# Kernel tuning notes

Measured on AMD Instinct MI355X. Metric: run time of the kernel, lower is better.

## Reference

```python
import jax, jax.numpy as jnp
import numpy as np

HEADS = 12
DIM = 768


def setup_inputs() -> dict:
    key = jax.random.key(0)
    ks = jax.random.split(key, 4)
    s = 0.02
    return {
        "x": jax.random.normal(ks[0], (8, 64, 64, DIM), dtype=jnp.float32),
        "w_qkv_h": jax.random.normal(ks[1], (DIM, 3 * DIM), dtype=jnp.float32) * s,
        "b_qkv_h": jnp.zeros((3 * DIM,), jnp.float32),
        "w_qkv_w": jax.random.normal(ks[2], (DIM, 3 * DIM), dtype=jnp.float32) * s,
        "b_qkv_w": jnp.zeros((3 * DIM,), jnp.float32),
        "w_proj": jax.random.normal(ks[3], (DIM, DIM), dtype=jnp.float32) * s,
        "b_proj": jnp.zeros((DIM,), jnp.float32),
    }


def _axial_attn(x_seq, w, b, heads, scale):
    # x_seq: [N, L, C]. Faithful to original torch code: q,k,v keep shape
    # [N, L, heads, hd]; matmul contracts hd, producing [N, L, heads, heads]
    # attention ACROSS HEADS at each position (no head permute in the source).
    N, L, C = x_seq.shape
    hd = C // heads
    qkv = (x_seq @ w + b).reshape(N, L, 3, heads, hd)
    q = qkv[:, :, 0] * scale
    k = qkv[:, :, 1]
    v = qkv[:, :, 2]
    attn = jax.nn.softmax(jnp.einsum('nlhd,nlgd->nlhg', q, k), axis=-1)
    out = jnp.einsum('nlhg,nlgd->nlhd', attn, v)
    return out.reshape(N, L, C)


def reference(x, w_qkv_h, b_qkv_h, w_qkv_w, b_qkv_w, w_proj, b_proj):
    B, H, W, C = x.shape
    scale = (C // HEADS) ** -0.5
    # H-axis pass: permute to [B, W, H, C], flatten batch*W
    x_h = jnp.transpose(x, (0, 2, 1, 3)).reshape(B * W, H, C)
    out_h = _axial_attn(x_h, w_qkv_h, b_qkv_h, HEADS, scale)
    out_h = jnp.transpose(out_h.reshape(B, W, H, C), (0, 2, 1, 3))
    # W-axis pass: flatten batch*H
    out_w = _axial_attn(x.reshape(B * H, W, C), w_qkv_w, b_qkv_w, HEADS, scale)
    out_w = out_w.reshape(B, H, W, C)
    # residual-style sum of the two axes, then output projection (dropout p=0)
    return (out_h + out_w) @ w_proj + b_proj
```

## Files before the change

### kernel.cpp

```cpp
#include <hip/hip_runtime.h>

typedef unsigned short u16;
typedef unsigned int u32;
typedef __attribute__((ext_vector_type(8))) short short8;
typedef __attribute__((ext_vector_type(4))) float f32x4;

#define DIMC 768
#define NQKV 2304
#define NPOS 32768
#define NKT 12

__device__ __forceinline__ float b2f(u16 u) {
    union { u32 i; float f; } c; c.i = ((u32)u) << 16; return c.f;
}
__device__ __forceinline__ u16 f2b(float f) {
    union { float f; u32 i; } c; c.f = f;
    u32 r = c.i + 0x7fffu + ((c.i >> 16) & 1u);
    return (u16)(r >> 16);
}

__device__ __forceinline__ void gl_lds16(const void* g, void* l) {
    __builtin_amdgcn_global_load_lds(
        (const __attribute__((address_space(1))) void*)g,
        (__attribute__((address_space(3))) void*)l, 16, 0, 0);
}

__global__ __launch_bounds__(256) void cvt_bf16(
    const float* __restrict__ in, u16* __restrict__ out, int n4)
{
    int i = blockIdx.x * 256 + threadIdx.x;
    if (i >= n4) return;
    float4 v = ((const float4*)in)[i];
    ushort4 o;
    o.x = f2b(v.x); o.y = f2b(v.y); o.z = f2b(v.z); o.w = f2b(v.w);
    ((ushort4*)out)[i] = o;
}

__global__ __launch_bounds__(256) void cvt_wT(
    const float* __restrict__ W0, const float* __restrict__ W1,
    const float* __restrict__ W2,
    u16* __restrict__ T0, u16* __restrict__ T1, u16* __restrict__ T2)
{
    const int z = blockIdx.z;
    const float* W = (z == 0) ? W0 : (z == 1) ? W1 : W2;
    u16* WT = (z == 0) ? T0 : (z == 1) ? T1 : T2;
    const int N = (z == 2) ? 768 : 2304;
    const int nb = blockIdx.x, kb = blockIdx.y;
    if (nb * 64 >= N) return;
    __shared__ u16 T[64][65];
    const int t = threadIdx.x, sr = t >> 2, sc = t & 3;
    {
        const float4* p = (const float4*)(W + (size_t)(kb * 64 + sr) * N + nb * 64 + sc * 16);
        float4 a0 = p[0], a1 = p[1], a2 = p[2], a3 = p[3];
        float vv[16] = {a0.x, a0.y, a0.z, a0.w, a1.x, a1.y, a1.z, a1.w,
                        a2.x, a2.y, a2.z, a2.w, a3.x, a3.y, a3.z, a3.w};
        #pragma unroll
        for (int i = 0; i < 16; ++i)
            T[sc * 16 + i][sr] = f2b(vv[i]);
    }
    __syncthreads();
    {
        u16 vv[16];
        #pragma unroll
        for (int i = 0; i < 16; ++i) vv[i] = T[sr][sc * 16 + i];
        uint4 p0, p1;
        p0.x = vv[0] | ((u32)vv[1] << 16);  p0.y = vv[2] | ((u32)vv[3] << 16);
        p0.z = vv[4] | ((u32)vv[5] << 16);  p0.w = vv[6] | ((u32)vv[7] << 16);
        p1.x = vv[8] | ((u32)vv[9] << 16);  p1.y = vv[10] | ((u32)vv[11] << 16);
        p1.z = vv[12] | ((u32)vv[13] << 16); p1.w = vv[14] | ((u32)vv[15] << 16);
        u16* q = WT + (size_t)(nb * 64 + sr) * DIMC + kb * 64 + sc * 16;
        *(uint4*)q = p0;
        *(uint4*)(q + 8) = p1;
    }
}


#define STAGE_A(buf, kt, ht) do {                                              \
    gl_lds16(aS + (size_t)((ht) * 128)      * DIMC + (size_t)(kt) * 64,        \
             &As[buf][(ht) * 8192 +        w * 512]);                          \
    gl_lds16(aS + (size_t)((ht) * 128 + 64) * DIMC + (size_t)(kt) * 64,        \
             &As[buf][(ht) * 8192 + 4096 + w * 512]);                          \
} while (0)

#define STAGE_B(buf, kt, ht) do {                                              \
    gl_lds16(bS + (size_t)((ht) * 128)      * DIMC + (size_t)(kt) * 64,        \
             &Bs[buf][(ht) * 8192 +        w * 512]);                          \
    gl_lds16(bS + (size_t)((ht) * 128 + 64) * DIMC + (size_t)(kt) * 64,        \
             &Bs[buf][(ht) * 8192 + 4096 + w * 512]);                          \
} while (0)

#define READ_A(base, hm) do {                                                  \
    _Pragma("unroll")                                                          \
    for (int i_ = 0; i_ < 4; ++i_) {                                           \
        const int row_ = (hm) * 128 + wm * 64 + i_ * 16 + lr;                  \
        _Pragma("unroll")                                                      \
        for (int ks_ = 0; ks_ < 2; ++ks_)                                      \
            af[i_][ks_] = *(const short8*)((base) + (row_ << 6) +              \
                              (((ks_ * 4 + lq) ^ (row_ & 7)) << 3));           \
    }                                                                          \
} while (0)

#define READ_B(dst, base, hn) do {                                             \
    _Pragma("unroll")                                                          \
    for (int j_ = 0; j_ < 2; ++j_) {                                           \
        const int row_ = (hn) * 128 + wn * 32 + j_ * 16 + lr;                  \
        _Pragma("unroll")                                                      \
        for (int ks_ = 0; ks_ < 2; ++ks_)                                      \
            (dst)[j_][ks_] = *(const short8*)((base) + (row_ << 6) +           \
                              (((ks_ * 4 + lq) ^ (row_ & 7)) << 3));           \
    }                                                                          \
} while (0)

#define MM(hm, hn, bsrc) do {                                                  \
    __builtin_amdgcn_s_setprio(1);                                             \
    _Pragma("unroll")                                                          \
    for (int i_ = 0; i_ < 4; ++i_)                                             \
        _Pragma("unroll")                                                      \
        for (int j_ = 0; j_ < 2; ++j_)                                         \
            _Pragma("unroll")                                                  \
            for (int ks_ = 0; ks_ < 2; ++ks_)                                  \
                acc[(hm) * 4 + i_][(hn) * 2 + j_] =                            \
                    __builtin_amdgcn_mfma_f32_16x16x32_bf16(                   \
                        af[i_][ks_], (bsrc)[j_][ks_],                          \
                        acc[(hm) * 4 + i_][(hn) * 2 + j_], 0, 0, 0);           \
    __builtin_amdgcn_s_setprio(0);                                             \
} while (0)

#define BAR() do {                                                             \
    __builtin_amdgcn_sched_barrier(0);                                         \
    __builtin_amdgcn_s_barrier();                                              \
    __builtin_amdgcn_sched_barrier(0);                                         \
} while (0)

#define KTILE(kt, S12, S34, VN) do {                                           \
    const int p_ = (kt) & 1, q_ = p_ ^ 1;                                      \
    const u16* Ab_ = As[p_];                                                   \
    const u16* Bb_ = Bs[p_];                                                   \
                                                             \
    READ_A(Ab_, 0);                                                            \
    READ_B(b0, Bb_, 0);                                                        \
    if (S12) STAGE_B(q_, (kt) + 1, 1);                                         \
    BAR();                                                                     \
    MM(0, 0, b0);                                                              \
                                                             \
    READ_B(b1, Bb_, 1);                                                        \
    if (S12) STAGE_A(q_, (kt) + 1, 1);                                         \
    BAR();                                                                     \
    MM(0, 1, b1);                                                              \
                                                             \
    READ_A(Ab_, 1);                                                            \
    if (S34) STAGE_A(p_, (kt) + 2, 0);                                         \
    BAR();                                                                     \
    MM(1, 0, b0);                                                              \
                                                             \
    if (S34) STAGE_B(p_, (kt) + 2, 0);                                         \
    __builtin_amdgcn_sched_barrier(0);                                         \
    asm volatile("s_waitcnt vmcnt(" VN ")" ::: "memory");                      \
    BAR();                                                                     \
    MM(1, 1, b1);                                                              \
} while (0)

__global__ __launch_bounds__(512, 2) void gemm256(
    const u16* __restrict__ A, const u16* __restrict__ BT,
    const float* __restrict__ bias, void* __restrict__ C,
    int ldn, int c_is_f32)
{
    __shared__ __align__(16) u16 As[2][256 * 64];
    __shared__ __align__(16) u16 Bs[2][256 * 64];

    const int t = threadIdx.x;
    const int w = t >> 6, l = t & 63;
    const int wm = w >> 2, wn = w & 3;
    const int lr = l & 15, lq = l >> 4;

    const int gx = (int)gridDim.x;
    const int nwg = gx * (int)gridDim.y;
    const int lin = (int)blockIdx.y * gx + (int)blockIdx.x;
    const int swz = (lin & 7) * (nwg >> 3) + (lin >> 3);
    const int by = swz / gx, bx = swz - by * gx;
    const int mBase = by * 256, nBase = bx * 256;

    const int srow = t >> 3;
    const int schk = (t & 7) ^ (srow & 7);
    const u16* aS = A  + (size_t)(mBase + srow) * DIMC + schk * 8;
    const u16* bS = BT + (size_t)(nBase + srow) * DIMC + schk * 8;

    f32x4 acc[8][4];
    #pragma unroll
    for (int i = 0; i < 8; ++i)
        #pragma unroll
        for (int j = 0; j < 4; ++j)
            acc[i][j] = (f32x4){0.f, 0.f, 0.f, 0.f};

    short8 af[4][2], b0[2][2], b1[2][2];

    STAGE_A(0, 0, 0); STAGE_B(0, 0, 0); STAGE_B(0, 0, 1); STAGE_A(0, 0, 1);
    STAGE_A(1, 1, 0); STAGE_B(1, 1, 0);
    __builtin_amdgcn_sched_barrier(0);
    asm volatile("s_waitcnt vmcnt(4)" ::: "memory");
    BAR();

    #pragma unroll 1
    for (int kt = 0; kt < NKT - 2; ++kt) { KTILE(kt, 1, 1, "4"); }
    { KTILE(NKT - 2, 1, 0, "0"); }
    { KTILE(NKT - 1, 0, 0, "0"); }

    #pragma unroll
    for (int hn = 0; hn < 2; ++hn)
        #pragma unroll
        for (int j = 0; j < 2; ++j) {
            const int col = nBase + hn * 128 + wn * 32 + j * 16 + lr;
            const float bb = bias[col];
            #pragma unroll
            for (int hm = 0; hm < 2; ++hm)
                #pragma unroll
                for (int i = 0; i < 4; ++i) {
                    const int row = mBase + hm * 128 + wm * 64 + i * 16 + lq * 4;
                    #pragma unroll
                    for (int rg = 0; rg < 4; ++rg) {
                        float v = acc[hm * 4 + i][hn * 2 + j][rg] + bb;
                        size_t idx = (size_t)(row + rg) * ldn + col;
                        if (c_is_f32) ((float*)C)[idx] = v;
                        else          ((u16*)C)[idx]   = f2b(v);
                    }
                }
        }
}

__global__ __launch_bounds__(256) void headattn(
    const u16* __restrict__ qkv, u16* __restrict__ sum, int accumulate)
{
    __shared__ u16 VtL[4][64 * 16];
    __shared__ u16 PL[4][16 * 16];
    const int t = threadIdx.x, wv = t >> 6, l = t & 63;
    const int p = blockIdx.x * 4 + wv;
    const u16* row = qkv + (size_t)p * NQKV;
    const int lr = l & 15, lq = l >> 4;
    u16* Vt = VtL[wv];
    u16* P  = PL[wv];

    short8 qa0 = *(const short8*)(row +       lr * 64 + lq * 8);
    short8 qa1 = *(const short8*)(row +       lr * 64 + lq * 8 + 32);
    short8 kb0 = *(const short8*)(row + 768 + lr * 64 + lq * 8);
    short8 kb1 = *(const short8*)(row + 768 + lr * 64 + lq * 8 + 32);

    *(uint2*)(Vt + l * 16 + 12) = (uint2){0u, 0u};
    {
        const int g = l >> 3, d0 = (l & 7) * 8;
        short8 v = *(const short8*)(row + 1536 + g * 64 + d0);
        #pragma unroll
        for (int i = 0; i < 8; ++i) Vt[(d0 + i) * 16 + g] = (u16)v[i];
        if (l < 32) {
            const int g2 = 8 + (l >> 3);
            short8 v2 = *(const short8*)(row + 1536 + g2 * 64 + d0);
            #pragma unroll
            for (int i = 0; i < 8; ++i) Vt[(d0 + i) * 16 + g2] = (u16)v2[i];
        }
    }

    f32x4 s = (f32x4){0.f, 0.f, 0.f, 0.f};
    s = __builtin_amdgcn_mfma_f32_16x16x32_bf16(qa0, kb0, s, 0, 0, 0);
    s = __builtin_amdgcn_mfma_f32_16x16x32_bf16(qa1, kb1, s, 0, 0, 0);

    #pragma unroll
    for (int rg = 0; rg < 4; ++rg) {
        float x = (lr < 12) ? s[rg] * 0.125f : -1e30f;
        float m = x;
        m = fmaxf(m, __shfl_xor(m, 1));
        m = fmaxf(m, __shfl_xor(m, 2));
        m = fmaxf(m, __shfl_xor(m, 4));
        m = fmaxf(m, __shfl_xor(m, 8));
        float e = (lr < 12) ? __expf(x - m) : 0.f;
        float ss = e;
        ss += __shfl_xor(ss, 1);
        ss += __shfl_xor(ss, 2);
        ss += __shfl_xor(ss, 4);
        ss += __shfl_xor(ss, 8);
        P[(lq * 4 + rg) * 16 + lr] = f2b(e / ss);
    }

    const short8 z8 = (short8){0, 0, 0, 0, 0, 0, 0, 0};
    short8 pa = z8;
    if (lq < 2) pa = *(const short8*)(P + lr * 16 + lq * 8);
    f32x4 o[4];
    #pragma unroll
    for (int c = 0; c < 4; ++c) {
        short8 vb = z8;
        if (lq < 2) vb = *(const short8*)(Vt + (c * 16 + lr) * 16 + lq * 8);
        f32x4 a0 = (f32x4){0.f, 0.f, 0.f, 0.f};
        o[c] = __builtin_amdgcn_mfma_f32_16x16x32_bf16(pa, vb, a0, 0, 0, 0);
    }

    if (lq < 3) {
        u16* orow = sum + (size_t)p * DIMC;
        #pragma unroll
        for (int c = 0; c < 4; ++c)
            #pragma unroll
            for (int rg = 0; rg < 4; ++rg) {
                const int idx = (lq * 4 + rg) * 64 + c * 16 + lr;
                float v = o[c][rg];
                if (accumulate) v += b2f(orow[idx]);
                orow[idx] = f2b(v);
            }
    }
}

extern "C" void kernel_launch(void* const* d_in, const int* in_sizes, int n_in,
                              void* d_out, int out_size, void* d_ws, size_t ws_size,
                              hipStream_t stream) {
    const float* x  = (const float*)d_in[0];
    const float* wh = (const float*)d_in[1];
    const float* bh = (const float*)d_in[2];
    const float* ww = (const float*)d_in[3];
    const float* bw = (const float*)d_in[4];
    const float* wp = (const float*)d_in[5];
    const float* bp = (const float*)d_in[6];
    float* out = (float*)d_out;

    u16* xb   = (u16*)d_ws;
    u16* whT  = xb   + 25165824;
    u16* wwT  = whT  + 1769472;
    u16* wpT  = wwT  + 1769472;
    u16* qkvb = wpT  + 589824;
    u16* sumb = qkvb + 75497472;

    cvt_bf16<<<24576, 256, 0, stream>>>(x, xb, 6291456);
    dim3 wg(36, 12, 3);
    cvt_wT<<<wg, 256, 0, stream>>>(wh, ww, wp, whT, wwT, wpT);

    dim3 gq(NQKV / 256, NPOS / 256);
    dim3 gp(DIMC / 256, NPOS / 256);

    gemm256<<<gq, 512, 0, stream>>>(xb, whT, bh, qkvb, NQKV, 0);
    headattn<<<NPOS / 4, 256, 0, stream>>>(qkvb, sumb, 0);
    gemm256<<<gq, 512, 0, stream>>>(xb, wwT, bw, qkvb, NQKV, 0);
    headattn<<<NPOS / 4, 256, 0, stream>>>(qkvb, sumb, 1);
    gemm256<<<gp, 512, 0, stream>>>(sumb, wpT, bp, out, DIMC, 1);
}
```

Measured before the change: 585.1 us.

## Fuse both axial attention passes into one kernel and prefetch GEMM fragments

The two per-position head-attention launches are merged into one kernel that reads both QKV buffers, sums both outputs in registers and writes the bf16 sum once. This removes the read-modify-write of the sum buffer and one launch. The P·V product now runs on VALU FMAs with shuffles instead of MFMA through LDS. The GEMM main loop double-buffers its A fragments and loads the next tile's A/B fragments during the last MFMA block, hiding LDS latency at the cost of more registers. A second QKV buffer is allocated, and the sum reuses the x bf16 buffer.

```diff
diff --git a/kernel.cpp b/kernel.cpp
--- a/kernel.cpp
+++ b/kernel.cpp
@@ -89,13 +89,13 @@
              &Bs[buf][(ht) * 8192 + 4096 + w * 512]);                          \
 } while (0)
 
-#define READ_A(base, hm) do {                                                  \
+#define READ_A(dst, base, hm) do {                                             \
     _Pragma("unroll")                                                          \
     for (int i_ = 0; i_ < 4; ++i_) {                                           \
         const int row_ = (hm) * 128 + wm * 64 + i_ * 16 + lr;                  \
         _Pragma("unroll")                                                      \
         for (int ks_ = 0; ks_ < 2; ++ks_)                                      \
-            af[i_][ks_] = *(const short8*)((base) + (row_ << 6) +              \
+            (dst)[i_][ks_] = *(const short8*)((base) + (row_ << 6) +           \
                               (((ks_ * 4 + lq) ^ (row_ & 7)) << 3));           \
     }                                                                          \
 } while (0)
@@ -111,7 +111,7 @@
     }                                                                          \
 } while (0)
 
-#define MM(hm, hn, bsrc) do {                                                  \
+#define MM(hm, hn, asrc, bsrc) do {                                            \
     __builtin_amdgcn_s_setprio(1);                                             \
     _Pragma("unroll")                                                          \
     for (int i_ = 0; i_ < 4; ++i_)                                             \
@@ -121,7 +121,7 @@
             for (int ks_ = 0; ks_ < 2; ++ks_)                                  \
                 acc[(hm) * 4 + i_][(hn) * 2 + j_] =                            \
                     __builtin_amdgcn_mfma_f32_16x16x32_bf16(                   \
-                        af[i_][ks_], (bsrc)[j_][ks_],                          \
+                        (asrc)[i_][ks_], (bsrc)[j_][ks_],                      \
                         acc[(hm) * 4 + i_][(hn) * 2 + j_], 0, 0, 0);           \
     __builtin_amdgcn_s_setprio(0);                                             \
 } while (0)
@@ -132,32 +132,29 @@
     __builtin_amdgcn_sched_barrier(0);                                         \
 } while (0)
 
-#define KTILE(kt, S12, S34, VN) do {                                           \
+#define KTILE(kt, S12, S34, SNEXT, VN) do {                                    \
     const int p_ = (kt) & 1, q_ = p_ ^ 1;                                      \
-    const u16* Ab_ = As[p_];                                                   \
-    const u16* Bb_ = Bs[p_];                                                   \
                                                              \
-    READ_A(Ab_, 0);                                                            \
-    READ_B(b0, Bb_, 0);                                                        \
     if (S12) STAGE_B(q_, (kt) + 1, 1);                                         \
+    READ_B(b1, Bs[p_], 1);                                                     \
     BAR();                                                                     \
-    MM(0, 0, b0);                                                              \
+    MM(0, 0, af_a, b0);                                                        \
                                                              \
-    READ_B(b1, Bb_, 1);                                                        \
     if (S12) STAGE_A(q_, (kt) + 1, 1);                                         \
+    READ_A(af_b, As[p_], 1);                                                   \
     BAR();                                                                     \
-    MM(0, 1, b1);                                                              \
+    MM(0, 1, af_a, b1);                                                        \
                                                              \
-    READ_A(Ab_, 1);                                                            \
     if (S34) STAGE_A(p_, (kt) + 2, 0);                                         \
     BAR();                                                                     \
-    MM(1, 0, b0);                                                              \
+    MM(1, 0, af_b, b0);                                                        \
                                                              \
     if (S34) STAGE_B(p_, (kt) + 2, 0);                                         \
     __builtin_amdgcn_sched_barrier(0);                                         \
     asm volatile("s_waitcnt vmcnt(" VN ")" ::: "memory");                      \
     BAR();                                                                     \
-    MM(1, 1, b1);                                                              \
+    if (SNEXT) { READ_A(af_a, As[q_], 0); READ_B(b0, Bs[q_], 0); }             \
+    MM(1, 1, af_b, b1);                                                        \
 } while (0)
 
 __global__ __launch_bounds__(512, 2) void gemm256(
@@ -192,18 +189,20 @@
         for (int j = 0; j < 4; ++j)
             acc[i][j] = (f32x4){0.f, 0.f, 0.f, 0.f};
 
-    short8 af[4][2], b0[2][2], b1[2][2];
+    short8 af_a[4][2], af_b[4][2], b0[2][2], b1[2][2];
 
     STAGE_A(0, 0, 0); STAGE_B(0, 0, 0); STAGE_B(0, 0, 1); STAGE_A(0, 0, 1);
     STAGE_A(1, 1, 0); STAGE_B(1, 1, 0);
     __builtin_amdgcn_sched_barrier(0);
     asm volatile("s_waitcnt vmcnt(4)" ::: "memory");
     BAR();
+    READ_A(af_a, As[0], 0);
+    READ_B(b0, Bs[0], 0);
 
     #pragma unroll 1
-    for (int kt = 0; kt < NKT - 2; ++kt) { KTILE(kt, 1, 1, "4"); }
-    { KTILE(NKT - 2, 1, 0, "0"); }
-    { KTILE(NKT - 1, 0, 0, "0"); }
+    for (int kt = 0; kt < NKT - 2; ++kt) { KTILE(kt, 1, 1, 1, "4"); }
+    { KTILE(NKT - 2, 1, 0, 1, "0"); }
+    { KTILE(NKT - 1, 0, 0, 0, "0"); }
 
     #pragma unroll
     for (int hn = 0; hn < 2; ++hn)
@@ -227,41 +226,14 @@
         }
 }
 
-__global__ __launch_bounds__(256) void headattn(
-    const u16* __restrict__ qkv, u16* __restrict__ sum, int accumulate)
-{
-    __shared__ u16 VtL[4][64 * 16];
-    __shared__ u16 PL[4][16 * 16];
-    const int t = threadIdx.x, wv = t >> 6, l = t & 63;
-    const int p = blockIdx.x * 4 + wv;
-    const u16* row = qkv + (size_t)p * NQKV;
-    const int lr = l & 15, lq = l >> 4;
-    u16* Vt = VtL[wv];
-    u16* P  = PL[wv];
-
-    short8 qa0 = *(const short8*)(row +       lr * 64 + lq * 8);
-    short8 qa1 = *(const short8*)(row +       lr * 64 + lq * 8 + 32);
-    short8 kb0 = *(const short8*)(row + 768 + lr * 64 + lq * 8);
-    short8 kb1 = *(const short8*)(row + 768 + lr * 64 + lq * 8 + 32);
-
-    *(uint2*)(Vt + l * 16 + 12) = (uint2){0u, 0u};
-    {
-        const int g = l >> 3, d0 = (l & 7) * 8;
-        short8 v = *(const short8*)(row + 1536 + g * 64 + d0);
-        #pragma unroll
-        for (int i = 0; i < 8; ++i) Vt[(d0 + i) * 16 + g] = (u16)v[i];
-        if (l < 32) {
-            const int g2 = 8 + (l >> 3);
-            short8 v2 = *(const short8*)(row + 1536 + g2 * 64 + d0);
-            #pragma unroll
-            for (int i = 0; i < 8; ++i) Vt[(d0 + i) * 16 + g2] = (u16)v2[i];
-        }
-    }
-
+__device__ __forceinline__ void attn_one(
+    short8 qa0, short8 qa1, short8 kb0, short8 kb1,
+    const u16* __restrict__ V, float* o, int lr, int l)
+{
     f32x4 s = (f32x4){0.f, 0.f, 0.f, 0.f};
     s = __builtin_amdgcn_mfma_f32_16x16x32_bf16(qa0, kb0, s, 0, 0, 0);
     s = __builtin_amdgcn_mfma_f32_16x16x32_bf16(qa1, kb1, s, 0, 0, 0);
-
+    float pp[4];
     #pragma unroll
     for (int rg = 0; rg < 4; ++rg) {
         float x = (lr < 12) ? s[rg] * 0.125f : -1e30f;
@@ -276,33 +248,62 @@
         ss += __shfl_xor(ss, 2);
         ss += __shfl_xor(ss, 4);
         ss += __shfl_xor(ss, 8);
-        P[(lq * 4 + rg) * 16 + lr] = f2b(e / ss);
-    }
-
-    const short8 z8 = (short8){0, 0, 0, 0, 0, 0, 0, 0};
-    short8 pa = z8;
-    if (lq < 2) pa = *(const short8*)(P + lr * 16 + lq * 8);
-    f32x4 o[4];
-    #pragma unroll
-    for (int c = 0; c < 4; ++c) {
-        short8 vb = z8;
-        if (lq < 2) vb = *(const short8*)(Vt + (c * 16 + lr) * 16 + lq * 8);
-        f32x4 a0 = (f32x4){0.f, 0.f, 0.f, 0.f};
-        o[c] = __builtin_amdgcn_mfma_f32_16x16x32_bf16(pa, vb, a0, 0, 0, 0);
-    }
-
-    if (lq < 3) {
-        u16* orow = sum + (size_t)p * DIMC;
-        #pragma unroll
-        for (int c = 0; c < 4; ++c)
-            #pragma unroll
-            for (int rg = 0; rg < 4; ++rg) {
-                const int idx = (lq * 4 + rg) * 64 + c * 16 + lr;
-                float v = o[c][rg];
-                if (accumulate) v += b2f(orow[idx]);
-                orow[idx] = f2b(v);
-            }
-    }
+        pp[rg] = e / ss;
+    }
+    #pragma unroll
+    for (int g = 0; g < 12; ++g) {
+        float vg = b2f(V[g * 64 + l]);
+        #pragma unroll
+        for (int h = 0; h < 12; ++h)
+            o[h] = fmaf(__shfl(pp[h & 3], (h >> 2) * 16 + g), vg, o[h]);
+    }
+}
+
+__global__ __launch_bounds__(256) void headattn2(
+    const u16* __restrict__ qkv1, const u16* __restrict__ qkv2,
+    u16* __restrict__ sum)
+{
+    __shared__ __align__(16) u16 VL[4][2][768];
+    const int t = threadIdx.x, wv = t >> 6, l = t & 63;
+    const int p = blockIdx.x * 4 + wv;
+    const u16* r1 = qkv1 + (size_t)p * NQKV;
+    const u16* r2 = qkv2 + (size_t)p * NQKV;
+    const int lr = l & 15;
+    const int fo = lr * 64 + (l >> 4) * 8;
+
+    short8 qa0_1 = *(const short8*)(r1 + fo);
+    short8 qa1_1 = *(const short8*)(r1 + fo + 32);
+    short8 kb0_1 = *(const short8*)(r1 + 768 + fo);
+    short8 kb1_1 = *(const short8*)(r1 + 768 + fo + 32);
+    short8 qa0_2 = *(const short8*)(r2 + fo);
+    short8 qa1_2 = *(const short8*)(r2 + fo + 32);
+    short8 kb0_2 = *(const short8*)(r2 + 768 + fo);
+    short8 kb1_2 = *(const short8*)(r2 + 768 + fo + 32);
+    short8 v1a = *(const short8*)(r1 + 1536 + l * 8);
+    short8 v2a = *(const short8*)(r2 + 1536 + l * 8);
+    short8 v1b, v2b;
+    if (l < 32) {
+        v1b = *(const short8*)(r1 + 1536 + 512 + l * 8);
+        v2b = *(const short8*)(r2 + 1536 + 512 + l * 8);
+    }
+    *(short8*)(&VL[wv][0][l * 8]) = v1a;
+    *(short8*)(&VL[wv][1][l * 8]) = v2a;
+    if (l < 32) {
+        *(short8*)(&VL[wv][0][512 + l * 8]) = v1b;
+        *(short8*)(&VL[wv][1][512 + l * 8]) = v2b;
+    }
+
+    float o[12];
+    #pragma unroll
+    for (int h = 0; h < 12; ++h) o[h] = 0.f;
+
+    attn_one(qa0_1, qa1_1, kb0_1, kb1_1, VL[wv][0], o, lr, l);
+    attn_one(qa0_2, qa1_2, kb0_2, kb1_2, VL[wv][1], o, lr, l);
+
+    u16* orow = sum + (size_t)p * DIMC;
+    #pragma unroll
+    for (int h = 0; h < 12; ++h)
+        orow[h * 64 + l] = f2b(o[h]);
 }
 
 extern "C" void kernel_launch(void* const* d_in, const int* in_sizes, int n_in,
@@ -318,11 +319,12 @@
     float* out = (float*)d_out;
 
     u16* xb   = (u16*)d_ws;
+    u16* sumb = xb;
     u16* whT  = xb   + 25165824;
     u16* wwT  = whT  + 1769472;
     u16* wpT  = wwT  + 1769472;
-    u16* qkvb = wpT  + 589824;
-    u16* sumb = qkvb + 75497472;
+    u16* qkv1 = wpT  + 589824;
+    u16* qkv2 = qkv1 + 75497472;
 
     cvt_bf16<<<24576, 256, 0, stream>>>(x, xb, 6291456);
     dim3 wg(36, 12, 3);
@@ -331,9 +333,8 @@
     dim3 gq(NQKV / 256, NPOS / 256);
     dim3 gp(DIMC / 256, NPOS / 256);
 
-    gemm256<<<gq, 512, 0, stream>>>(xb, whT, bh, qkvb, NQKV, 0);
-    headattn<<<NPOS / 4, 256, 0, stream>>>(qkvb, sumb, 0);
-    gemm256<<<gq, 512, 0, stream>>>(xb, wwT, bw, qkvb, NQKV, 0);
-    headattn<<<NPOS / 4, 256, 0, stream>>>(qkvb, sumb, 1);
+    gemm256<<<gq, 512, 0, stream>>>(xb, whT, bh, qkv1, NQKV, 0);
+    gemm256<<<gq, 512, 0, stream>>>(xb, wwT, bw, qkv2, NQKV, 0);
+    headattn2<<<NPOS / 4, 256, 0, stream>>>(qkv1, qkv2, sumb);
     gemm256<<<gp, 512, 0, stream>>>(sumb, wpT, bp, out, DIMC, 1);
 }
```

Measured after the change: 733.8 us. 25.4% more time.
